# Kernel tuning notes

Hardware: AMD Instinct MI355X
Metric: run time of the kernel (lower is better)

## Reference

```python
import jax, jax.numpy as jnp
import numpy as np

B_SZ, N_IN, N_CTX, UNITS, RANK = 4096, 4096, 512, 4096, 256


def setup_inputs() -> dict:
    key = jax.random.key(0)
    ks = jax.random.split(key, 8)
    inputs = jax.random.normal(ks[0], (B_SZ, N_IN), dtype=jnp.float32)
    context = jax.random.normal(ks[1], (B_SZ, N_CTX), dtype=jnp.float32)
    # Orthogonal-ish init approximated by scaled normals (math-equivalent shapes)
    U = jax.random.normal(ks[2], (N_IN, RANK), dtype=jnp.float32) / np.sqrt(N_IN)
    S = jax.random.uniform(ks[3], (RANK,), dtype=jnp.float32, minval=0.5, maxval=1.5)
    V = jax.random.normal(ks[4], (UNITS, RANK), dtype=jnp.float32) / np.sqrt(UNITS)
    W = jax.random.normal(ks[5], (N_CTX, RANK), dtype=jnp.float32) / np.sqrt(N_CTX)
    B = jnp.zeros((RANK,), dtype=jnp.float32)
    bias = jnp.zeros((UNITS,), dtype=jnp.float32)
    return {"inputs": inputs, "context": context, "U": U, "S": S, "V": V, "W": W, "B": B, "bias": bias}


def reference(inputs, context, U, S, V, W, B, bias):
    # chi[b,r] = sigmoid(context @ W + B)
    chi = jax.nn.sigmoid(context @ W + B)                  # [B, R]
    # Original: kernel[b,n,m] = sum_r U[n,r]*S[r]*chi[b,r]*V[m,r];
    # out[b,m] = sum_n x[b,n]*kernel[b,n,m]. Algebraically equal to:
    t = (inputs @ U) * (S * chi)                           # [B, R]
    out = t @ V.T + bias                                   # first '+ self.bias'
    out = out + bias                                       # 'outputs += self.bias' (use_bias=True)
    return jax.nn.relu(out)
```

## Files before the change

kernel.cpp:

```cpp
#include <hip/hip_runtime.h>

#define B_SZ 4096
#define N_IN 4096
#define N_CTX 512
#define UNITS 4096
#define RANK 256
#define ZSPLIT 8

typedef __attribute__((ext_vector_type(8))) __bf16 bf16x8;
typedef __attribute__((ext_vector_type(4))) float f32x4;
typedef __attribute__((ext_vector_type(8))) unsigned short ushort8;

__device__ __forceinline__ unsigned short f2bf(float f) {
    __bf16 h = (__bf16)f;
    return __builtin_bit_cast(unsigned short, h);
}
__device__ __forceinline__ float bf2f(unsigned short h) {
    return __uint_as_float(((unsigned int)h) << 16);
}
__device__ __forceinline__ void gload_lds16(const unsigned short* g, unsigned short* l) {
    __builtin_amdgcn_global_load_lds(
        (const __attribute__((address_space(1))) unsigned int*)g,
        (__attribute__((address_space(3))) unsigned int*)l, 16, 0, 0);
}
__device__ __forceinline__ bf16x8 ldfrag(const unsigned short* p) {
    ushort8 t = *(const ushort8*)p;
    return __builtin_bit_cast(bf16x8, t);
}

__global__ void prep(const float* __restrict__ U, const float* __restrict__ W,
                     const float* __restrict__ V,
                     unsigned short* __restrict__ UT, unsigned short* __restrict__ WT,
                     unsigned short* __restrict__ Vb) {
    __shared__ unsigned short t[64][66];
    int bid = blockIdx.x, tid = threadIdx.x;
    if (bid < 288) {
        const float* src; unsigned short* dst; int R, C, rb, cb;
        if (bid < 256) { src = U; dst = UT; R = N_IN; C = RANK; rb = (bid & 63) * 64; cb = (bid >> 6) * 64; }
        else { int b = bid - 256; src = W; dst = WT; R = N_CTX; C = RANK; rb = (b & 7) * 64; cb = (b >> 3) * 64; }
        int r = tid >> 4, c4 = (tid & 15) * 4;
        for (int i = 0; i < 4; i++) {
            float4 v = *(const float4*)(src + (size_t)(rb + r + i * 16) * C + cb + c4);
            t[r + i * 16][c4 + 0] = f2bf(v.x);
            t[r + i * 16][c4 + 1] = f2bf(v.y);
            t[r + i * 16][c4 + 2] = f2bf(v.z);
            t[r + i * 16][c4 + 3] = f2bf(v.w);
        }
        __syncthreads();
        int c = tid >> 3, r8 = (tid & 7) * 8;
        for (int j = 0; j < 2; j++) {
            int cc = c + j * 32;
            ushort8 o;
            for (int k = 0; k < 8; k++) o[k] = t[r8 + k][cc];
            *(ushort8*)(dst + (size_t)(cb + cc) * R + rb + r8) = o;
        }
    } else {
        size_t base = (size_t)(bid - 288) * 2048 + (size_t)tid * 8;
        float4 a = *(const float4*)(V + base);
        float4 b = *(const float4*)(V + base + 4);
        ushort8 o = { f2bf(a.x), f2bf(a.y), f2bf(a.z), f2bf(a.w),
                      f2bf(b.x), f2bf(b.y), f2bf(b.z), f2bf(b.w) };
        *(ushort8*)(Vb + base) = o;
    }
}


__launch_bounds__(256, 4)
__global__ void k1_chi(const float* __restrict__ ctx, const unsigned short* __restrict__ WT,
                       const float* __restrict__ S, const float* __restrict__ Bb,
                       unsigned short* __restrict__ Schi) {
    __shared__ unsigned short As[32 * 64];
    __shared__ unsigned short Bs[64 * 64];
    int tid = threadIdx.x, w = tid >> 6, lane = tid & 63;
    int ln15 = lane & 15, quad = lane >> 4;
    int wr = w >> 1, wc = w & 1;
    int tm = blockIdx.y * 32, tn = blockIdx.x * 64;
    f32x4 acc2[2] = {};
    int arow = tid >> 3, acs = tid & 7;
    const float* ag = ctx + (size_t)(tm + arow) * N_CTX + acs * 8;
    unsigned short* al = As + arow * 64 + (acs ^ (arow & 7)) * 8;
    int bl8 = lane >> 3, bcs = lane & 7;
    int bgc = (bcs ^ bl8) * 8;
    for (int kt = 0; kt < 8; kt++) {
        int k0 = kt * 64;
        for (int c = 0; c < 2; c++) {
            int row = w * 16 + c * 8 + bl8;
            gload_lds16(WT + (size_t)(tn + row) * N_CTX + k0 + bgc, Bs + row * 64 + bcs * 8);
        }
        {
            float4 v0 = *(const float4*)(ag + k0);
            float4 v1 = *(const float4*)(ag + k0 + 4);
            ushort8 a8 = { f2bf(v0.x), f2bf(v0.y), f2bf(v0.z), f2bf(v0.w),
                           f2bf(v1.x), f2bf(v1.y), f2bf(v1.z), f2bf(v1.w) };
            *(ushort8*)al = a8;
        }
        __syncthreads();
        for (int kh = 0; kh < 2; kh++) {
            int ch = kh * 4 + quad;
            bf16x8 af = ldfrag(As + (wr * 16 + ln15) * 64 + (ch ^ (ln15 & 7)) * 8);
            for (int j = 0; j < 2; j++) {
                int row = wc * 32 + j * 16 + ln15;
                bf16x8 bfr = ldfrag(Bs + row * 64 + (ch ^ (ln15 & 7)) * 8);
                acc2[j] = __builtin_amdgcn_mfma_f32_16x16x32_bf16(af, bfr, acc2[j], 0, 0, 0);
            }
        }
        __syncthreads();
    }
    for (int j = 0; j < 2; j++) {
        int col = tn + wc * 32 + j * 16 + ln15;
        float sv = S[col], bv = Bb[col];
        for (int r = 0; r < 4; r++) {
            int row = tm + wr * 16 + quad * 4 + r;
            float x = acc2[j][r] + bv;
            float chi = sv / (1.f + __expf(-x));
            Schi[(size_t)row * RANK + col] = f2bf(chi);
        }
    }
}

__launch_bounds__(256, 2)
__global__ void k2_t0(const float* __restrict__ X, const unsigned short* __restrict__ UT,
                      unsigned short* __restrict__ T0p) {
    __shared__ unsigned short As[64 * 64];
    __shared__ unsigned short Bs[256 * 64];
    int tid = threadIdx.x, w = tid >> 6, lane = tid & 63;
    int ln15 = lane & 15, quad = lane >> 4;
    int wr = w >> 1, wc = w & 1;
    int tm = blockIdx.y * 64;
    int kbase = blockIdx.z * (N_IN / ZSPLIT);
    f32x4 acc[2][8] = {};
    int arow = tid >> 2, acs0 = (tid & 3) * 2;
    const float* ag = X + (size_t)(tm + arow) * N_IN + kbase + acs0 * 8;
    unsigned short* al0 = As + arow * 64 + ((acs0 + 0) ^ (arow & 7)) * 8;
    unsigned short* al1 = As + arow * 64 + ((acs0 + 1) ^ (arow & 7)) * 8;
    int bl8 = lane >> 3, bcs = lane & 7;
    int bgc = (bcs ^ bl8) * 8;
    for (int kt = 0; kt < (N_IN / ZSPLIT) / 64; kt++) {
        int k0 = kt * 64;
        for (int c = 0; c < 8; c++) {
            int row = w * 64 + c * 8 + bl8;
            gload_lds16(UT + (size_t)row * N_IN + kbase + k0 + bgc, Bs + row * 64 + bcs * 8);
        }
        {
            float4 v0 = *(const float4*)(ag + k0);
            float4 v1 = *(const float4*)(ag + k0 + 4);
            float4 u0 = *(const float4*)(ag + k0 + 8);
            float4 u1 = *(const float4*)(ag + k0 + 12);
            ushort8 a8 = { f2bf(v0.x), f2bf(v0.y), f2bf(v0.z), f2bf(v0.w),
                           f2bf(v1.x), f2bf(v1.y), f2bf(v1.z), f2bf(v1.w) };
            ushort8 b8 = { f2bf(u0.x), f2bf(u0.y), f2bf(u0.z), f2bf(u0.w),
                           f2bf(u1.x), f2bf(u1.y), f2bf(u1.z), f2bf(u1.w) };
            *(ushort8*)al0 = a8;
            *(ushort8*)al1 = b8;
        }
        __syncthreads();
        for (int kh = 0; kh < 2; kh++) {
            int ch = kh * 4 + quad;
            int sw = (ch ^ (ln15 & 7)) * 8;
            bf16x8 af[2], bfr[8];
            for (int i = 0; i < 2; i++)
                af[i] = ldfrag(As + (wr * 32 + i * 16 + ln15) * 64 + sw);
            for (int j = 0; j < 8; j++)
                bfr[j] = ldfrag(Bs + (wc * 128 + j * 16 + ln15) * 64 + sw);
            for (int i = 0; i < 2; i++)
                for (int j = 0; j < 8; j++)
                    acc[i][j] = __builtin_amdgcn_mfma_f32_16x16x32_bf16(af[i], bfr[j], acc[i][j], 0, 0, 0);
        }
        __syncthreads();
    }
    unsigned short* P = T0p + (size_t)blockIdx.z * B_SZ * RANK;
    for (int i = 0; i < 2; i++)
        for (int j = 0; j < 8; j++) {
            int col = wc * 128 + j * 16 + ln15;
            for (int r = 0; r < 4; r++) {
                int row = tm + wr * 32 + i * 16 + quad * 4 + r;
                P[(size_t)row * RANK + col] = f2bf(acc[i][j][r]);
            }
        }
}

__global__ void e_red(const unsigned short* __restrict__ T0p, const unsigned short* __restrict__ Schi,
                      unsigned short* __restrict__ T) {
    int i = blockIdx.x * 256 + threadIdx.x;
    const size_t stride = (size_t)B_SZ * RANK;
    float a[8] = {};
    for (int z = 0; z < ZSPLIT; z++) {
        ushort8 p = *(const ushort8*)(T0p + z * stride + (size_t)i * 8);
        for (int k = 0; k < 8; k++) a[k] += bf2f(p[k]);
    }
    ushort8 s = *(const ushort8*)(Schi + (size_t)i * 8);
    ushort8 o;
    for (int k = 0; k < 8; k++) o[k] = f2bf(a[k] * bf2f(s[k]));
    *(ushort8*)(T + (size_t)i * 8) = o;
}

__launch_bounds__(256, 3)
__global__ void k3_out(const unsigned short* __restrict__ T, const unsigned short* __restrict__ Vb,
                       const float* __restrict__ bias, float* __restrict__ out) {
    __shared__ unsigned short As[128 * 64];
    __shared__ unsigned short Bs[128 * 64];
    int tid = threadIdx.x, w = tid >> 6, lane = tid & 63;
    int ln15 = lane & 15, quad = lane >> 4;
    int wr = w >> 1, wc = w & 1;
    int tn = blockIdx.x * 128, tm = blockIdx.y * 128;
    f32x4 acc[4][4] = {};
    int bl8 = lane >> 3, bcs = lane & 7;
    int bgc = (bcs ^ bl8) * 8;
    for (int kt = 0; kt < RANK / 64; kt++) {
        int k0 = kt * 64;
        for (int c = 0; c < 4; c++) {
            int row = w * 32 + c * 8 + bl8;
            gload_lds16(T + (size_t)(tm + row) * RANK + k0 + bgc, As + row * 64 + bcs * 8);
        }
        for (int c = 0; c < 4; c++) {
            int row = w * 32 + c * 8 + bl8;
            gload_lds16(Vb + (size_t)(tn + row) * RANK + k0 + bgc, Bs + row * 64 + bcs * 8);
        }
        __syncthreads();
        for (int kh = 0; kh < 2; kh++) {
            int ch = kh * 4 + quad;
            int sw = (ch ^ (ln15 & 7)) * 8;
            bf16x8 af[4], bfr[4];
            for (int i = 0; i < 4; i++)
                af[i] = ldfrag(As + (wr * 64 + i * 16 + ln15) * 64 + sw);
            for (int j = 0; j < 4; j++)
                bfr[j] = ldfrag(Bs + (wc * 64 + j * 16 + ln15) * 64 + sw);
            for (int i = 0; i < 4; i++)
                for (int j = 0; j < 4; j++)
                    acc[i][j] = __builtin_amdgcn_mfma_f32_16x16x32_bf16(af[i], bfr[j], acc[i][j], 0, 0, 0);
        }
        __syncthreads();
    }
    for (int j = 0; j < 4; j++) {
        int col = tn + wc * 64 + j * 16 + ln15;
        float bv = 2.f * bias[col];
        for (int i = 0; i < 4; i++)
            for (int r = 0; r < 4; r++) {
                int row = tm + wr * 64 + i * 16 + quad * 4 + r;
                float v = acc[i][j][r] + bv;
                out[(size_t)row * UNITS + col] = fmaxf(v, 0.f);
            }
    }
}

extern "C" void kernel_launch(void* const* d_in, const int* in_sizes, int n_in,
                              void* d_out, int out_size, void* d_ws, size_t ws_size,
                              hipStream_t stream) {
    (void)in_sizes; (void)n_in; (void)out_size; (void)ws_size;
    const float* inputs  = (const float*)d_in[0];
    const float* context = (const float*)d_in[1];
    const float* U       = (const float*)d_in[2];
    const float* S       = (const float*)d_in[3];
    const float* V       = (const float*)d_in[4];
    const float* W       = (const float*)d_in[5];
    const float* Bb      = (const float*)d_in[6];
    const float* bias    = (const float*)d_in[7];
    float* out = (float*)d_out;

    char* ws = (char*)d_ws;
    size_t o = 0;
    unsigned short* UT   = (unsigned short*)(ws + o); o += (size_t)RANK * N_IN * 2;
    unsigned short* WT   = (unsigned short*)(ws + o); o += (size_t)RANK * N_CTX * 2;
    unsigned short* Vb   = (unsigned short*)(ws + o); o += (size_t)UNITS * RANK * 2;
    unsigned short* Schi = (unsigned short*)(ws + o); o += (size_t)B_SZ * RANK * 2;
    unsigned short* T    = (unsigned short*)(ws + o); o += (size_t)B_SZ * RANK * 2;
    unsigned short* T0p  = (unsigned short*)(ws + o); o += (size_t)ZSPLIT * B_SZ * RANK * 2;

    prep<<<800, 256, 0, stream>>>(U, W, V, UT, WT, Vb);
    k2_t0<<<dim3(1, B_SZ / 64, ZSPLIT), 256, 0, stream>>>(inputs, UT, T0p);
    k1_chi<<<dim3(RANK / 64, B_SZ / 32), 256, 0, stream>>>(context, WT, S, Bb, Schi);
    e_red<<<(B_SZ * RANK) / (256 * 8), 256, 0, stream>>>(T0p, Schi, T);
    k3_out<<<dim3(UNITS / 128, B_SZ / 128), 256, 0, stream>>>(T, Vb, bias, out);
}
```

Baseline: 171.1 us.

## Pre-convert inputs to bf16 in prep and retile k2 with async LDS loads

The fp32 input matrix is now converted to bf16 in the prep kernel and written to a workspace buffer. The k2 GEMM then loads both operands straight into LDS with global_load_lds, using 128x128 tiles and a 4x4 MFMA accumulator layout. ZSPLIT is doubled to 16 so the grid still has enough blocks. The cost is an extra full pass over the 64MB input (read fp32, write bf16, read again) and twice as much partial-sum traffic for e_red, in exchange for removing the in-loop fp32 loads and conversions from k2.

Result: slower. 193.0 us (+12.8%).

```diff
diff --git a/kernel.cpp b/kernel.cpp
--- a/kernel.cpp
+++ b/kernel.cpp
@@ -5,7 +5,7 @@
 #define N_CTX 512
 #define UNITS 4096
 #define RANK 256
-#define ZSPLIT 8
+#define ZSPLIT 16
 
 typedef __attribute__((ext_vector_type(8))) __bf16 bf16x8;
 typedef __attribute__((ext_vector_type(4))) float f32x4;
@@ -29,9 +29,9 @@
 }
 
 __global__ void prep(const float* __restrict__ U, const float* __restrict__ W,
-                     const float* __restrict__ V,
+                     const float* __restrict__ V, const float* __restrict__ X,
                      unsigned short* __restrict__ UT, unsigned short* __restrict__ WT,
-                     unsigned short* __restrict__ Vb) {
+                     unsigned short* __restrict__ Vb, unsigned short* __restrict__ Xb) {
     __shared__ unsigned short t[64][66];
     int bid = blockIdx.x, tid = threadIdx.x;
     if (bid < 288) {
@@ -54,13 +54,25 @@
             for (int k = 0; k < 8; k++) o[k] = t[r8 + k][cc];
             *(ushort8*)(dst + (size_t)(cb + cc) * R + rb + r8) = o;
         }
-    } else {
+    } else if (bid < 800) {
         size_t base = (size_t)(bid - 288) * 2048 + (size_t)tid * 8;
         float4 a = *(const float4*)(V + base);
         float4 b = *(const float4*)(V + base + 4);
         ushort8 o = { f2bf(a.x), f2bf(a.y), f2bf(a.z), f2bf(a.w),
                       f2bf(b.x), f2bf(b.y), f2bf(b.z), f2bf(b.w) };
         *(ushort8*)(Vb + base) = o;
+    } else {
+        size_t base = (size_t)(bid - 800) * 4096 + (size_t)tid * 16;
+        float4 a = *(const float4*)(X + base);
+        float4 b = *(const float4*)(X + base + 4);
+        float4 c = *(const float4*)(X + base + 8);
+        float4 d = *(const float4*)(X + base + 12);
+        ushort8 o0 = { f2bf(a.x), f2bf(a.y), f2bf(a.z), f2bf(a.w),
+                       f2bf(b.x), f2bf(b.y), f2bf(b.z), f2bf(b.w) };
+        ushort8 o1 = { f2bf(c.x), f2bf(c.y), f2bf(c.z), f2bf(c.w),
+                       f2bf(d.x), f2bf(d.y), f2bf(d.z), f2bf(d.w) };
+        *(ushort8*)(Xb + base) = o0;
+        *(ushort8*)(Xb + base + 8) = o1;
     }
 }
 
@@ -118,65 +130,50 @@
     }
 }
 
-__launch_bounds__(256, 2)
-__global__ void k2_t0(const float* __restrict__ X, const unsigned short* __restrict__ UT,
+__launch_bounds__(256, 3)
+__global__ void k2_t0(const unsigned short* __restrict__ Xb, const unsigned short* __restrict__ UT,
                       unsigned short* __restrict__ T0p) {
-    __shared__ unsigned short As[64 * 64];
-    __shared__ unsigned short Bs[256 * 64];
+    __shared__ unsigned short As[128 * 64];
+    __shared__ unsigned short Bs[128 * 64];
     int tid = threadIdx.x, w = tid >> 6, lane = tid & 63;
     int ln15 = lane & 15, quad = lane >> 4;
     int wr = w >> 1, wc = w & 1;
-    int tm = blockIdx.y * 64;
+    int tm = blockIdx.y * 128, tn = blockIdx.x * 128;
     int kbase = blockIdx.z * (N_IN / ZSPLIT);
-    f32x4 acc[2][8] = {};
-    int arow = tid >> 2, acs0 = (tid & 3) * 2;
-    const float* ag = X + (size_t)(tm + arow) * N_IN + kbase + acs0 * 8;
-    unsigned short* al0 = As + arow * 64 + ((acs0 + 0) ^ (arow & 7)) * 8;
-    unsigned short* al1 = As + arow * 64 + ((acs0 + 1) ^ (arow & 7)) * 8;
+    f32x4 acc[4][4] = {};
     int bl8 = lane >> 3, bcs = lane & 7;
     int bgc = (bcs ^ bl8) * 8;
     for (int kt = 0; kt < (N_IN / ZSPLIT) / 64; kt++) {
         int k0 = kt * 64;
-        for (int c = 0; c < 8; c++) {
-            int row = w * 64 + c * 8 + bl8;
-            gload_lds16(UT + (size_t)row * N_IN + kbase + k0 + bgc, Bs + row * 64 + bcs * 8);
-        }
-        {
-            float4 v0 = *(const float4*)(ag + k0);
-            float4 v1 = *(const float4*)(ag + k0 + 4);
-            float4 u0 = *(const float4*)(ag + k0 + 8);
-            float4 u1 = *(const float4*)(ag + k0 + 12);
-            ushort8 a8 = { f2bf(v0.x), f2bf(v0.y), f2bf(v0.z), f2bf(v0.w),
-                           f2bf(v1.x), f2bf(v1.y), f2bf(v1.z), f2bf(v1.w) };
-            ushort8 b8 = { f2bf(u0.x), f2bf(u0.y), f2bf(u0.z), f2bf(u0.w),
-                           f2bf(u1.x), f2bf(u1.y), f2bf(u1.z), f2bf(u1.w) };
-            *(ushort8*)al0 = a8;
-            *(ushort8*)al1 = b8;
+        for (int c = 0; c < 4; c++) {
+            int row = w * 32 + c * 8 + bl8;
+            gload_lds16(Xb + (size_t)(tm + row) * N_IN + kbase + k0 + bgc, As + row * 64 + bcs * 8);
+            gload_lds16(UT + (size_t)(tn + row) * N_IN + kbase + k0 + bgc, Bs + row * 64 + bcs * 8);
         }
         __syncthreads();
         for (int kh = 0; kh < 2; kh++) {
             int ch = kh * 4 + quad;
             int sw = (ch ^ (ln15 & 7)) * 8;
-            bf16x8 af[2], bfr[8];
-            for (int i = 0; i < 2; i++)
-                af[i] = ldfrag(As + (wr * 32 + i * 16 + ln15) * 64 + sw);
-            for (int j = 0; j < 8; j++)
-                bfr[j] = ldfrag(Bs + (wc * 128 + j * 16 + ln15) * 64 + sw);
-            for (int i = 0; i < 2; i++)
-                for (int j = 0; j < 8; j++)
+            bf16x8 af[4], bfr[4];
+            for (int i = 0; i < 4; i++)
+                af[i] = ldfrag(As + (wr * 64 + i * 16 + ln15) * 64 + sw);
+            for (int j = 0; j < 4; j++)
+                bfr[j] = ldfrag(Bs + (wc * 64 + j * 16 + ln15) * 64 + sw);
+            for (int i = 0; i < 4; i++)
+                for (int j = 0; j < 4; j++)
                     acc[i][j] = __builtin_amdgcn_mfma_f32_16x16x32_bf16(af[i], bfr[j], acc[i][j], 0, 0, 0);
         }
         __syncthreads();
     }
     unsigned short* P = T0p + (size_t)blockIdx.z * B_SZ * RANK;
-    for (int i = 0; i < 2; i++)
-        for (int j = 0; j < 8; j++) {
-            int col = wc * 128 + j * 16 + ln15;
+    for (int j = 0; j < 4; j++) {
+        int col = tn + wc * 64 + j * 16 + ln15;
+        for (int i = 0; i < 4; i++)
             for (int r = 0; r < 4; r++) {
-                int row = tm + wr * 32 + i * 16 + quad * 4 + r;
+                int row = tm + wr * 64 + i * 16 + quad * 4 + r;
                 P[(size_t)row * RANK + col] = f2bf(acc[i][j][r]);
             }
-        }
+    }
 }
 
 __global__ void e_red(const unsigned short* __restrict__ T0p, const unsigned short* __restrict__ Schi,
@@ -211,9 +208,6 @@
         for (int c = 0; c < 4; c++) {
             int row = w * 32 + c * 8 + bl8;
             gload_lds16(T + (size_t)(tm + row) * RANK + k0 + bgc, As + row * 64 + bcs * 8);
-        }
-        for (int c = 0; c < 4; c++) {
-            int row = w * 32 + c * 8 + bl8;
             gload_lds16(Vb + (size_t)(tn + row) * RANK + k0 + bgc, Bs + row * 64 + bcs * 8);
         }
         __syncthreads();
@@ -262,12 +256,13 @@
     unsigned short* UT   = (unsigned short*)(ws + o); o += (size_t)RANK * N_IN * 2;
     unsigned short* WT   = (unsigned short*)(ws + o); o += (size_t)RANK * N_CTX * 2;
     unsigned short* Vb   = (unsigned short*)(ws + o); o += (size_t)UNITS * RANK * 2;
+    unsigned short* Xb   = (unsigned short*)(ws + o); o += (size_t)B_SZ * N_IN * 2;
     unsigned short* Schi = (unsigned short*)(ws + o); o += (size_t)B_SZ * RANK * 2;
     unsigned short* T    = (unsigned short*)(ws + o); o += (size_t)B_SZ * RANK * 2;
     unsigned short* T0p  = (unsigned short*)(ws + o); o += (size_t)ZSPLIT * B_SZ * RANK * 2;
 
-    prep<<<800, 256, 0, stream>>>(U, W, V, UT, WT, Vb);
-    k2_t0<<<dim3(1, B_SZ / 64, ZSPLIT), 256, 0, stream>>>(inputs, UT, T0p);
+    prep<<<4896, 256, 0, stream>>>(U, W, V, inputs, UT, WT, Vb, Xb);
+    k2_t0<<<dim3(RANK / 128, B_SZ / 128, ZSPLIT), 256, 0, stream>>>(Xb, UT, T0p);
     k1_chi<<<dim3(RANK / 64, B_SZ / 32), 256, 0, stream>>>(context, WT, S, Bb, Schi);
     e_red<<<(B_SZ * RANK) / (256 * 8), 256, 0, stream>>>(T0p, Schi, T);
     k3_out<<<dim3(UNITS / 128, B_SZ / 128), 256, 0, stream>>>(T, Vb, bias, out);
```
